# Performance work log

Measured on AMD Instinct MI355X. Metric: run time of the kernel, lower is better.

The kernel has to match this reference:

```python
import jax, jax.numpy as jnp
import numpy as np

SRC_SIZE = 1024
TGT_SIZE = 1024
ATT_SIZE = 1024
S, T, B = 1024, 1024, 32


def setup_inputs() -> dict:
    key = jax.random.key(0)
    k1, k2, k3, k4 = jax.random.split(key, 4)
    source = jax.random.normal(k1, (S, B, SRC_SIZE), dtype=jnp.float32)
    target = jax.random.normal(k2, (T, B, TGT_SIZE), dtype=jnp.float32)
    # nn.Linear(in, out, bias=False): weight shape (out, in), y = x @ W.T
    scale1 = 1.0 / np.sqrt(SRC_SIZE)
    scale2 = 1.0 / np.sqrt(TGT_SIZE)
    W1 = jax.random.uniform(k3, (ATT_SIZE, SRC_SIZE), dtype=jnp.float32, minval=-scale1, maxval=scale1)
    W2 = jax.random.uniform(k4, (ATT_SIZE, TGT_SIZE), dtype=jnp.float32, minval=-scale2, maxval=scale2)
    return {"source": source, "target": target, "W1": W1, "W2": W2}


def reference(source, target, W1, W2):
    # Transform into attention space: (S,B,A) and (T,B,A)
    ts = jnp.einsum('sbd,ad->sba', source, W1)
    tt = jnp.einsum('tbd,ad->tba', target, W2)
    # Multiplicative scores: (S,T,B) = sum_a ts[s,b,a]*tt[t,b,a]
    scores = jnp.einsum('sba,tba->stb', ts, tt)
    # Softmax over source positions (axis 0)
    weights = jax.nn.softmax(scores, axis=0)  # (S,T,B)
    # Attention vectors: (T,B,src_size) = sum_s weights[s,t,b]*source[s,b,d]
    return jnp.einsum('stb,sbd->tbd', weights, source)
```

## Files before the change

kernel.cpp:

```cpp
#include <hip/hip_runtime.h>
#include <hip/hip_bf16.h>

typedef unsigned short ushort_t;
typedef _Float16 half_t;
typedef __attribute__((ext_vector_type(8))) _Float16 half8;
typedef __attribute__((ext_vector_type(4))) _Float16 half4;
typedef __attribute__((ext_vector_type(4))) float floatx4;
typedef __attribute__((ext_vector_type(4))) float f32x4;

#define DEVFN static __device__ __forceinline__

DEVFN void gll16(const void* g, void* l) {
    __builtin_amdgcn_global_load_lds(
        (const __attribute__((address_space(1))) unsigned int*)g,
        (__attribute__((address_space(3))) unsigned int*)l, 16, 0, 0);
}

__global__ __launch_bounds__(256) void cvt_f16(
    const float* __restrict__ in, half_t* __restrict__ out, int n4)
{
    int i = blockIdx.x * 256 + threadIdx.x;
    if (i >= n4) return;
    floatx4 v = ((const floatx4*)in)[i];
    half4 h;
#pragma unroll
    for (int j = 0; j < 4; j++) h[j] = (half_t)v[j];
    ((half4*)out)[i] = h;
}

__global__ __launch_bounds__(256) void transpose_src_f16(
    const float* __restrict__ src, half_t* __restrict__ srcT)
{
    __shared__ float tile[32][33];
    int s0 = blockIdx.x << 5, d0 = blockIdx.y << 5, b = blockIdx.z;
    int t = threadIdx.x;
    int si = t >> 3, dj = (t & 7) << 2;
    floatx4 v = *(const floatx4*)&src[((size_t)(s0 + si) * 32 + b) * 1024 + d0 + dj];
    tile[si][dj + 0] = v[0]; tile[si][dj + 1] = v[1];
    tile[si][dj + 2] = v[2]; tile[si][dj + 3] = v[3];
    __syncthreads();
    int di = t >> 3, sj = (t & 7) << 2;
    half4 o;
#pragma unroll
    for (int q = 0; q < 4; q++) o[q] = (half_t)tile[sj + q][di];
    *(half4*)&srcT[((size_t)b * 1024 + d0 + di) * 1024 + s0 + sj] = o;
}

template <bool OUT_F16>
__global__ __launch_bounds__(256, 2) void gemm_f16(
    const half_t* __restrict__ A, const half_t* __restrict__ B,
    void* __restrict__ Cv,
    int lda, int ldb, int ldc, int K,
    long long bA, long long bB, long long bC,
    int gx, int gy)
{
    __shared__ half_t sA[4096], sB[4096];
    int nwg = gridDim.x;
    int bid = blockIdx.x;
    int sw = (bid & 7) * (nwg >> 3) + (bid >> 3);
    int x = sw % gx;
    int r1 = sw / gx;
    int y = r1 % gy;
    int z = r1 / gy;

    int t = threadIdx.x, lane = t & 63, w = t >> 6;
    int m0 = y << 7, n0 = x << 7;
    size_t zA = (size_t)bA * z, zB = (size_t)bB * z, zC = (size_t)bC * z;
    const half_t* pA = A + zA + (size_t)m0 * lda;
    const half_t* pB = B + zB + (size_t)n0 * ldb;

    f32x4 acc[4][4];
#pragma unroll
    for (int m = 0; m < 4; m++)
#pragma unroll
        for (int n = 0; n < 4; n++) acc[m][n] = (f32x4){0.f, 0.f, 0.f, 0.f};

    int rb = (w >> 1) << 6, cb = (w & 1) << 6, fr = lane & 15, ko = (lane >> 4) << 3;

    for (int k0 = 0; k0 < K; k0 += 32) {
#pragma unroll
        for (int i = 0; i < 2; i++) {
            int e = ((w << 1) + i) << 9;
            int el = e + lane * 8;
            int r = el >> 5, c = el & 31;
            gll16(pA + (size_t)r * lda + k0 + c, sA + e);
            gll16(pB + (size_t)r * ldb + k0 + c, sB + e);
        }
        __syncthreads();

        half8 ah[4], bh[4];
#pragma unroll
        for (int f = 0; f < 4; f++) {
            ah[f] = *(const half8*)&sA[(rb + f * 16 + fr) * 32 + ko];
            bh[f] = *(const half8*)&sB[(cb + f * 16 + fr) * 32 + ko];
        }
#pragma unroll
        for (int m = 0; m < 4; m++)
#pragma unroll
            for (int n = 0; n < 4; n++)
                acc[m][n] = __builtin_amdgcn_mfma_f32_16x16x32_f16(ah[m], bh[n], acc[m][n], 0, 0, 0);
        __syncthreads();
    }

    int r0 = rb + ((lane >> 4) << 2);
    int c0 = cb + fr;
#pragma unroll
    for (int m = 0; m < 4; m++)
#pragma unroll
        for (int n = 0; n < 4; n++)
#pragma unroll
            for (int j = 0; j < 4; j++) {
                size_t idx = zC + (size_t)(m0 + r0 + m * 16 + j) * ldc + (n0 + c0 + n * 16);
                if constexpr (OUT_F16)
                    ((half_t*)Cv)[idx] = (half_t)acc[m][n][j];
                else
                    ((float*)Cv)[idx] = acc[m][n][j];
            }
}

__global__ __launch_bounds__(256) void softmax_k(
    const float* __restrict__ sc, half_t* __restrict__ wt)
{
    size_t row = blockIdx.x;
    const floatx4* p = (const floatx4*)(sc + row * 1024);
    int t = threadIdx.x, lane = t & 63, w = t >> 6;
    floatx4 v = p[t];
    float m = fmaxf(fmaxf(v[0], v[1]), fmaxf(v[2], v[3]));
#pragma unroll
    for (int o = 1; o < 64; o <<= 1) m = fmaxf(m, __shfl_xor(m, o));
    __shared__ float red[8];
    if (lane == 0) red[w] = m;
    __syncthreads();
    m = fmaxf(fmaxf(red[0], red[1]), fmaxf(red[2], red[3]));
    floatx4 e;
#pragma unroll
    for (int j = 0; j < 4; j++) e[j] = __expf(v[j] - m);
    float s = e[0] + e[1] + e[2] + e[3];
#pragma unroll
    for (int o = 1; o < 64; o <<= 1) s += __shfl_xor(s, o);
    if (lane == 0) red[4 + w] = s;
    __syncthreads();
    s = red[4] + red[5] + red[6] + red[7];
    float inv = 1.0f / s;
    half4 o4;
#pragma unroll
    for (int j = 0; j < 4; j++) o4[j] = (half_t)(e[j] * inv);
    ((half4*)(wt + row * 1024))[t] = o4;
}

extern "C" void kernel_launch(void* const* d_in, const int* in_sizes, int n_in,
                              void* d_out, int out_size, void* d_ws, size_t ws_size,
                              hipStream_t stream)
{
    const float* src = (const float*)d_in[0];
    const float* tgt = (const float*)d_in[1];
    const float* W1  = (const float*)d_in[2];
    const float* W2  = (const float*)d_in[3];
    float* out = (float*)d_out;

    char* ws = (char*)d_ws;
    const size_t MB = 1024ull * 1024ull;
    half_t* srcH  = (half_t*)(ws);
    half_t* tgtH  = (half_t*)(ws + 64  * MB);
    half_t* tsH   = (half_t*)(ws + 128 * MB);
    half_t* ttH   = (half_t*)(ws + 192 * MB);
    half_t* srcT  = (half_t*)(ws + 256 * MB);
    float*  scores= (float*) (ws + 320 * MB);
    half_t* w1h   = (half_t*)(ws + 448 * MB);
    half_t* w2h   = (half_t*)(ws + 450 * MB);
    half_t* wts   = srcH;

    cvt_f16<<<32768, 256, 0, stream>>>(src, srcH, 8388608);
    cvt_f16<<<32768, 256, 0, stream>>>(tgt, tgtH, 8388608);
    cvt_f16<<<1024, 256, 0, stream>>>(W1, w1h, 262144);
    cvt_f16<<<1024, 256, 0, stream>>>(W2, w2h, 262144);
    transpose_src_f16<<<dim3(32, 32, 32), 256, 0, stream>>>(src, srcT);

    gemm_f16<true><<<2048, 256, 0, stream>>>(srcH, w1h, tsH,
        1024, 1024, 1024, 1024, 0ll, 0ll, 0ll, 8, 256);
    gemm_f16<true><<<2048, 256, 0, stream>>>(tgtH, w2h, ttH,
        1024, 1024, 1024, 1024, 0ll, 0ll, 0ll, 8, 256);

    gemm_f16<false><<<2048, 256, 0, stream>>>(ttH, tsH, scores,
        32768, 32768, 1024, 1024, 1024ll, 1024ll, 1024ll * 1024ll, 8, 8);

    softmax_k<<<32768, 256, 0, stream>>>(scores, wts);

    gemm_f16<false><<<2048, 256, 0, stream>>>(wts, srcT, out,
        1024, 1024, 32768, 1024, 1024ll * 1024ll, 1024ll * 1024ll, 1024ll, 8, 8);
}
```

Baseline: 782.3 us.

## Use 256x256 double-buffered pipelined GEMM and fuse source fp16 conversion into transpose

Replaces the 128x128 single-buffered GEMM with a 512-thread 256x256 tile kernel. It double-buffers K=64 slabs in 128KB of LDS and interleaves async global-to-LDS loads with MFMA phases, using explicit waitcnt, barriers and setprio. This raises arithmetic intensity and hides load latency behind compute. Separately, the transpose kernel now also writes the row-major fp16 copy of source, which removes one full conversion pass over source. The cost is higher register and LDS pressure, which limits occupancy to one workgroup per CU, and only 512 workgroups per GEMM.

```diff
diff --git a/kernel.cpp b/kernel.cpp
--- a/kernel.cpp
+++ b/kernel.cpp
@@ -1,7 +1,6 @@
 #include <hip/hip_runtime.h>
 #include <hip/hip_bf16.h>
 
-typedef unsigned short ushort_t;
 typedef _Float16 half_t;
 typedef __attribute__((ext_vector_type(8))) _Float16 half8;
 typedef __attribute__((ext_vector_type(4))) _Float16 half4;
@@ -15,6 +14,14 @@
         (const __attribute__((address_space(1))) unsigned int*)g,
         (__attribute__((address_space(3))) unsigned int*)l, 16, 0, 0);
 }
+DEVFN f32x4 mfma16(half8 a, half8 b, f32x4 c) {
+    return __builtin_amdgcn_mfma_f32_16x16x32_f16(a, b, c, 0, 0, 0);
+}
+DEVFN void lgkm0() { asm volatile("s_waitcnt lgkmcnt(0)" ::: "memory"); __builtin_amdgcn_sched_barrier(0); }
+DEVFN void vm0()   { asm volatile("s_waitcnt vmcnt(0)"   ::: "memory"); __builtin_amdgcn_sched_barrier(0); }
+DEVFN void vm2()   { asm volatile("s_waitcnt vmcnt(2)"   ::: "memory"); __builtin_amdgcn_sched_barrier(0); }
+DEVFN void vm4()   { asm volatile("s_waitcnt vmcnt(4)"   ::: "memory"); __builtin_amdgcn_sched_barrier(0); }
+DEVFN void bar()   { __builtin_amdgcn_s_barrier(); __builtin_amdgcn_sched_barrier(0); }
 
 __global__ __launch_bounds__(256) void cvt_f16(
     const float* __restrict__ in, half_t* __restrict__ out, int n4)
@@ -29,7 +36,7 @@
 }
 
 __global__ __launch_bounds__(256) void transpose_src_f16(
-    const float* __restrict__ src, half_t* __restrict__ srcT)
+    const float* __restrict__ src, half_t* __restrict__ srcT, half_t* __restrict__ srcH)
 {
     __shared__ float tile[32][33];
     int s0 = blockIdx.x << 5, d0 = blockIdx.y << 5, b = blockIdx.z;
@@ -38,6 +45,10 @@
     floatx4 v = *(const floatx4*)&src[((size_t)(s0 + si) * 32 + b) * 1024 + d0 + dj];
     tile[si][dj + 0] = v[0]; tile[si][dj + 1] = v[1];
     tile[si][dj + 2] = v[2]; tile[si][dj + 3] = v[3];
+    half4 hv;
+#pragma unroll
+    for (int j = 0; j < 4; j++) hv[j] = (half_t)v[j];
+    *(half4*)&srcH[((size_t)(s0 + si) * 32 + b) * 1024 + d0 + dj] = hv;
     __syncthreads();
     int di = t >> 3, sj = (t & 7) << 2;
     half4 o;
@@ -47,74 +58,150 @@
 }
 
 template <bool OUT_F16>
-__global__ __launch_bounds__(256, 2) void gemm_f16(
+__global__ __launch_bounds__(512, 2) void gemm256(
     const half_t* __restrict__ A, const half_t* __restrict__ B,
     void* __restrict__ Cv,
     int lda, int ldb, int ldc, int K,
     long long bA, long long bB, long long bC,
     int gx, int gy)
 {
-    __shared__ half_t sA[4096], sB[4096];
-    int nwg = gridDim.x;
-    int bid = blockIdx.x;
-    int sw = (bid & 7) * (nwg >> 3) + (bid >> 3);
-    int x = sw % gx;
-    int r1 = sw / gx;
-    int y = r1 % gy;
-    int z = r1 / gy;
-
-    int t = threadIdx.x, lane = t & 63, w = t >> 6;
-    int m0 = y << 7, n0 = x << 7;
-    size_t zA = (size_t)bA * z, zB = (size_t)bB * z, zC = (size_t)bC * z;
-    const half_t* pA = A + zA + (size_t)m0 * lda;
-    const half_t* pB = B + zB + (size_t)n0 * ldb;
-
-    f32x4 acc[4][4];
-#pragma unroll
-    for (int m = 0; m < 4; m++)
+    __shared__ char lds[131072];
+    const int nwg = gridDim.x;
+    const int bid = blockIdx.x;
+    const int sw = (bid & 7) * (nwg >> 3) + (bid >> 3);
+    const int x = sw % gx;
+    const int r1 = sw / gx;
+    const int y = r1 % gy;
+    const int z = r1 / gy;
+
+    const int t = threadIdx.x, lane = t & 63, w = t >> 6;
+    const int wr = w >> 2, wc = w & 3;
+    const int m0 = y << 8, n0 = x << 8;
+    const half_t* pA = A + (size_t)bA * z + (size_t)m0 * lda;
+    const half_t* pB = B + (size_t)bB * z + (size_t)n0 * ldb;
+
+    int srow[2], scol[2];
+#pragma unroll
+    for (int i = 0; i < 2; i++) {
+        int slot = (w << 7) + (i << 6) + lane;
+        srow[i] = slot >> 2;
+        scol[i] = (slot & 3) << 3;
+    }
+    const unsigned stOff = (unsigned)((w << 7) << 4);
+
+    const int lr = lane & 15, q = lane >> 4;
+    const unsigned aRd = (unsigned)((((wr << 7) + lr) << 6) + (q << 4));
+    const unsigned bRd = 65536u + (unsigned)((((wc << 6) + lr) << 6) + (q << 4));
+
+    f32x4 acc[8][4];
+#pragma unroll
+    for (int m = 0; m < 8; m++)
 #pragma unroll
         for (int n = 0; n < 4; n++) acc[m][n] = (f32x4){0.f, 0.f, 0.f, 0.f};
 
-    int rb = (w >> 1) << 6, cb = (w & 1) << 6, fr = lane & 15, ko = (lane >> 4) << 3;
-
-    for (int k0 = 0; k0 < K; k0 += 32) {
-#pragma unroll
-        for (int i = 0; i < 2; i++) {
-            int e = ((w << 1) + i) << 9;
-            int el = e + lane * 8;
-            int r = el >> 5, c = el & 31;
-            gll16(pA + (size_t)r * lda + k0 + c, sA + e);
-            gll16(pB + (size_t)r * ldb + k0 + c, sB + e);
-        }
-        __syncthreads();
-
-        half8 ah[4], bh[4];
-#pragma unroll
-        for (int f = 0; f < 4; f++) {
-            ah[f] = *(const half8*)&sA[(rb + f * 16 + fr) * 32 + ko];
-            bh[f] = *(const half8*)&sB[(cb + f * 16 + fr) * 32 + ko];
-        }
-#pragma unroll
-        for (int m = 0; m < 4; m++)
-#pragma unroll
-            for (int n = 0; n < 4; n++)
-                acc[m][n] = __builtin_amdgcn_mfma_f32_16x16x32_f16(ah[m], bh[n], acc[m][n], 0, 0, 0);
-        __syncthreads();
+    auto stA = [&](int nb, int kh, int kc) {
+#pragma unroll
+        for (int i = 0; i < 2; i++)
+            gll16(pA + (size_t)srow[i] * lda + (kc + kh * 32 + scol[i]),
+                  lds + (nb << 15) + (kh << 14) + stOff + (i << 10));
+    };
+    auto stB = [&](int nb, int kh, int kc) {
+#pragma unroll
+        for (int i = 0; i < 2; i++)
+            gll16(pB + (size_t)srow[i] * ldb + (kc + kh * 32 + scol[i]),
+                  lds + 65536 + (nb << 15) + (kh << 14) + stOff + (i << 10));
+    };
+
+    stA(0, 0, 0); stA(0, 1, 0); stB(0, 0, 0); stB(0, 1, 0);
+    vm2();
+    bar();
+
+    half8 av[8], bv[2], bv2[2];
+    const int NT = K >> 6;
+    for (int tt = 0; tt < NT; ++tt) {
+        const int buf = tt & 1, nb = buf ^ 1;
+        const bool st = (tt + 1 < NT);
+        const int kn = (tt + 1) << 6;
+        const unsigned base0 = (unsigned)(buf << 15);
+        const unsigned base1 = base0 + 16384u;
+
+#pragma unroll
+        for (int m = 0; m < 8; m++) av[m] = *(const half8*)(lds + base0 + aRd + m * 1024);
+#pragma unroll
+        for (int n = 0; n < 2; n++) bv[n] = *(const half8*)(lds + base0 + bRd + n * 1024);
+        if (st) stA(nb, 0, kn);
+        bar();
+        lgkm0();
+        __builtin_amdgcn_s_setprio(1);
+#pragma unroll
+        for (int m = 0; m < 8; m++) {
+            acc[m][0] = mfma16(av[m], bv[0], acc[m][0]);
+            acc[m][1] = mfma16(av[m], bv[1], acc[m][1]);
+        }
+        __builtin_amdgcn_s_setprio(0);
+        bar();
+
+#pragma unroll
+        for (int n = 0; n < 2; n++) bv2[n] = *(const half8*)(lds + base0 + bRd + (2 + n) * 1024);
+        if (st) stA(nb, 1, kn);
+        bar();
+        lgkm0();
+        __builtin_amdgcn_s_setprio(1);
+#pragma unroll
+        for (int m = 0; m < 8; m++) {
+            acc[m][2] = mfma16(av[m], bv2[0], acc[m][2]);
+            acc[m][3] = mfma16(av[m], bv2[1], acc[m][3]);
+        }
+        __builtin_amdgcn_s_setprio(0);
+        if (st) vm4(); else vm0();
+        bar();
+
+#pragma unroll
+        for (int m = 0; m < 8; m++) av[m] = *(const half8*)(lds + base1 + aRd + m * 1024);
+#pragma unroll
+        for (int n = 0; n < 2; n++) bv[n] = *(const half8*)(lds + base1 + bRd + n * 1024);
+        if (st) stB(nb, 0, kn);
+        bar();
+        lgkm0();
+        __builtin_amdgcn_s_setprio(1);
+#pragma unroll
+        for (int m = 0; m < 8; m++) {
+            acc[m][0] = mfma16(av[m], bv[0], acc[m][0]);
+            acc[m][1] = mfma16(av[m], bv[1], acc[m][1]);
+        }
+        __builtin_amdgcn_s_setprio(0);
+        bar();
+
+#pragma unroll
+        for (int n = 0; n < 2; n++) bv2[n] = *(const half8*)(lds + base1 + bRd + (2 + n) * 1024);
+        if (st) stB(nb, 1, kn);
+        bar();
+        lgkm0();
+        __builtin_amdgcn_s_setprio(1);
+#pragma unroll
+        for (int m = 0; m < 8; m++) {
+            acc[m][2] = mfma16(av[m], bv2[0], acc[m][2]);
+            acc[m][3] = mfma16(av[m], bv2[1], acc[m][3]);
+        }
+        __builtin_amdgcn_s_setprio(0);
+        if (st) vm2();
+        bar();
     }
 
-    int r0 = rb + ((lane >> 4) << 2);
-    int c0 = cb + fr;
-#pragma unroll
-    for (int m = 0; m < 4; m++)
-#pragma unroll
-        for (int n = 0; n < 4; n++)
+    const size_t zC = (size_t)bC * z;
+    const int r0 = m0 + (wr << 7) + (q << 2);
+    const int c0 = n0 + (wc << 6) + lr;
+#pragma unroll
+    for (int m = 0; m < 8; m++)
+#pragma unroll
+        for (int fn = 0; fn < 4; fn++)
 #pragma unroll
             for (int j = 0; j < 4; j++) {
-                size_t idx = zC + (size_t)(m0 + r0 + m * 16 + j) * ldc + (n0 + c0 + n * 16);
+                size_t idx = zC + (size_t)(r0 + m * 16 + j) * ldc + (c0 + fn * 16);
                 if constexpr (OUT_F16)
-                    ((half_t*)Cv)[idx] = (half_t)acc[m][n][j];
+                    ((half_t*)Cv)[idx] = (half_t)acc[m][fn][j];
                 else
-                    ((float*)Cv)[idx] = acc[m][n][j];
+                    ((float*)Cv)[idx] = acc[m][fn][j];
             }
 }
 
@@ -170,22 +257,21 @@
     half_t* w2h   = (half_t*)(ws + 450 * MB);
     half_t* wts   = srcH;
 
-    cvt_f16<<<32768, 256, 0, stream>>>(src, srcH, 8388608);
     cvt_f16<<<32768, 256, 0, stream>>>(tgt, tgtH, 8388608);
     cvt_f16<<<1024, 256, 0, stream>>>(W1, w1h, 262144);
     cvt_f16<<<1024, 256, 0, stream>>>(W2, w2h, 262144);
-    transpose_src_f16<<<dim3(32, 32, 32), 256, 0, stream>>>(src, srcT);
-
-    gemm_f16<true><<<2048, 256, 0, stream>>>(srcH, w1h, tsH,
-        1024, 1024, 1024, 1024, 0ll, 0ll, 0ll, 8, 256);
-    gemm_f16<true><<<2048, 256, 0, stream>>>(tgtH, w2h, ttH,
-        1024, 1024, 1024, 1024, 0ll, 0ll, 0ll, 8, 256);
-
-    gemm_f16<false><<<2048, 256, 0, stream>>>(ttH, tsH, scores,
-        32768, 32768, 1024, 1024, 1024ll, 1024ll, 1024ll * 1024ll, 8, 8);
+    transpose_src_f16<<<dim3(32, 32, 32), 256, 0, stream>>>(src, srcT, srcH);
+
+    gemm256<true><<<512, 512, 0, stream>>>(srcH, w1h, tsH,
+        1024, 1024, 1024, 1024, 0ll, 0ll, 0ll, 4, 128);
+    gemm256<true><<<512, 512, 0, stream>>>(tgtH, w2h, ttH,
+        1024, 1024, 1024, 1024, 0ll, 0ll, 0ll, 4, 128);
+
+    gemm256<false><<<512, 512, 0, stream>>>(ttH, tsH, scores,
+        32768, 32768, 1024, 1024, 1024ll, 1024ll, 1024ll * 1024ll, 4, 4);
 
     softmax_k<<<32768, 256, 0, stream>>>(scores, wts);
 
-    gemm_f16<false><<<2048, 256, 0, stream>>>(wts, srcT, out,
-        1024, 1024, 32768, 1024, 1024ll * 1024ll, 1024ll * 1024ll, 1024ll, 8, 8);
-}
+    gemm256<false><<<512, 512, 0, stream>>>(wts, srcT, out,
+        1024, 1024, 32768, 1024, 1024ll * 1024ll, 1024ll * 1024ll, 1024ll, 4, 4);
+}
```

Result: faster. 707.7 us (-9.5%).
